# Kernel optimization log

Hardware: AMD Instinct MI355X
Metric: run time of the kernel (lower is better)

The kernel has to match this reference:

```python
import jax, jax.numpy as jnp
import numpy as np

B, N, DIM = 4, 1024, 1024
H, DH, ORDER = 16, 64, 3
MAXREL = 64
INNER = H * DH
VOCAB = 2 * MAXREL + 1
SCALE = DH ** -0.5
TOPK = int(0.25 * N)  # topk_ratio=0.25 default when top_k is None


def setup_inputs() -> dict:
    key = jax.random.key(0)
    ks = jax.random.split(key, 8)
    s = 0.02
    return {
        "x": jax.random.normal(ks[0], (B, N, DIM), jnp.float32),
        "Wqkv": jax.random.normal(ks[1], (3 * INNER, DIM), jnp.float32) * s,
        "bqkv": jnp.zeros((3 * INNER,), jnp.float32),
        "Wout": jax.random.normal(ks[2], (DIM, INNER), jnp.float32) * s,
        "bout": jnp.zeros((DIM,), jnp.float32),
        "rel_k_emb": jax.random.normal(ks[3], (VOCAB, DH), jnp.float32) * s,
        "rel_v_emb": jax.random.normal(ks[4], (VOCAB, DH), jnp.float32) * s,
        "alphas_raw": jax.random.normal(ks[5], (ORDER, H), jnp.float32) * 0.5,
    }


def reference(x, Wqkv, bqkv, Wout, bout, rel_k_emb, rel_v_emb, alphas_raw):
    b, n, _ = x.shape
    qkv = x @ Wqkv.T + bqkv  # [b, n, 3*inner]
    q, k, v = jnp.split(qkv, 3, axis=-1)
    to_heads = lambda t: t.reshape(b, n, H, DH).transpose(0, 2, 1, 3)  # b h n d
    q, k, v = to_heads(q), to_heads(k), to_heads(v)

    scores = jnp.einsum('bhid,bhjd->bhij', q, k) * SCALE

    # relative position bias on keys
    coords = jnp.arange(n)
    dist = jnp.clip(coords[:, None] - coords[None, :], -MAXREL, MAXREL) + MAXREL  # [n, n]
    rel_k = rel_k_emb[dist]  # [n, n, d]
    scores = scores + jnp.einsum('bhid,ijd->bhij', q, rel_k)

    # top-k thresholding per query row
    top_vals = jax.lax.top_k(scores, TOPK)[0]
    threshold = top_vals[..., -1:]
    scores = jnp.where(scores < threshold, -jnp.inf, scores)

    attn = jax.nn.softmax(scores, axis=-1)  # [b, h, n, n]

    rel_v = rel_v_emb[dist]  # [n, n, d]
    alphas = jax.nn.sigmoid(alphas_raw)  # [order, h]

    # monomial-basis polynomial filter: res = sum_i alpha_i * A^(i+1) V (+ relV term at i=0)
    res = jnp.zeros_like(v)
    v_curr = v
    for i in range(ORDER):
        a_v = jnp.einsum('bhij,bhjd->bhid', attn, v_curr)
        if i == 0:
            a_v = a_v + jnp.einsum('bhij,ijd->bhid', attn, rel_v)
        v_curr = a_v
        res = res + alphas[i][None, :, None, None] * v_curr

    out = res.transpose(0, 2, 1, 3).reshape(b, n, INNER)
    return out @ Wout.T + bout
```

## Files before the change

### kernel.cpp

```cpp
#include <hip/hip_runtime.h>

typedef unsigned short u16;
typedef unsigned int   u32;
typedef unsigned long long u64;
typedef __bf16 bf16x8 __attribute__((ext_vector_type(8)));
typedef float  floatx4 __attribute__((ext_vector_type(4)));

#define DEV static __device__ __forceinline__

DEV u16 f2bf(float f){ u32 x = __float_as_uint(f); return (u16)((x + 0x7fffu + ((x>>16)&1u)) >> 16); }
DEV float bf2f(u16 h){ return __uint_as_float(((u32)h)<<16); }
DEV u32 cvt_pk_bf16(float a, float b){ u32 r; asm("v_cvt_pk_bf16_f32 %0, %1, %2" : "=v"(r) : "v"(a), "v"(b)); return r; }

DEV void load_lds16(const u16* g, u16* l){
  __builtin_amdgcn_global_load_lds((const __attribute__((address_space(1))) u32*)g,
                                   (__attribute__((address_space(3))) u32*)l, 16, 0, 0);
}

DEV u32 unswz64(u32 p){
  u32 r0 = ((p>>6) ^ (p>>8)) & 1u;
  u32 b4 = ((p>>4) & 1u) ^ r0;
  u32 b5 = ((p>>5) ^ (p>>7)) & 1u;
  return (p & ~0x70u) | (b4<<4) | (b5<<5) | (r0<<6);
}
DEV bf16x8 ldfrag(const u16* base, int row, int lane){
  u32 off = ((u32)row<<6) + (((u32)lane>>4)<<4);
  off ^= (u32)(row&7)<<4;
  return *(const bf16x8*)((const char*)base + off);
}

template<int BM, int BN, int MODE>
__global__ __launch_bounds__(256) void gemm_bt(
    const u16* __restrict__ A, const u16* __restrict__ Bm, float* __restrict__ C,
    const float* __restrict__ bias, int K, int lda, int ldb, int ldc, int ncmax,
    long long sA, long long sB, long long sC,
    u16* __restrict__ vout, float* __restrict__ resb, const float* __restrict__ araw,
    int order, int accum)
{
  constexpr int BK = 32;
  constexpr int MT = BM/32;
  constexpr int NT = (BN/2)/16;
  __shared__ u16 smem[8704];
  u16* As = smem;
  u16* Bs = smem + BM*BK;

  const int tid = threadIdx.x, wid = tid>>6, lane = tid&63;
  const int z = blockIdx.z;
  const int m0 = blockIdx.y * BM, n0 = blockIdx.x * BN;
  const u16* Ab = A + (long long)z*sA;
  const u16* Bb = Bm + (long long)z*sB;

  const u32 g = unswz64((u32)tid*16);
  const int srow = g>>6, schunk = (g&63)>>1;
  const u16* ga0 = Ab + (long long)(m0 + srow)*lda + schunk;
  const u16* gb0 = Bb + (long long)(n0 + srow)*ldb + schunk;

  u16* lA0 = As + (wid*16)*BK;
  u16* lB0 = Bs + (wid*16)*BK;

  const int wm = wid>>1, wn = wid&1;
  const int lr = lane&15, lq = lane>>4;

  floatx4 acc[MT][NT] = {};

  for (int k = 0; k < K; k += BK) {
    __syncthreads();
    load_lds16(ga0 + k, lA0);
    load_lds16(gb0 + k, lB0);
    __syncthreads();
    bf16x8 af[MT];
#pragma unroll
    for (int mt=0; mt<MT; ++mt)
      af[mt] = ldfrag(As, wm*(BM/2) + mt*16 + lr, lane);
#pragma unroll
    for (int nt=0; nt<NT; ++nt) {
      bf16x8 bfr = ldfrag(Bs, wn*(BN/2) + nt*16 + lr, lane);
#pragma unroll
      for (int mt=0; mt<MT; ++mt)
        acc[mt][nt] = __builtin_amdgcn_mfma_f32_16x16x32_bf16(af[mt], bfr, acc[mt][nt], 0, 0, 0);
    }
  }

  if constexpr (MODE == 0) {
    float* Cb = C + (long long)z*sC;
#pragma unroll
    for (int nt=0; nt<NT; ++nt) {
      const int col = n0 + wn*(BN/2) + nt*16 + lr;
      if (col < ncmax) {
        const float bv = bias ? bias[col] : 0.f;
#pragma unroll
        for (int mt=0; mt<MT; ++mt) {
#pragma unroll
          for (int r=0; r<4; ++r) {
            const int row = m0 + wm*(BM/2) + mt*16 + lq*4 + r;
            Cb[(long long)row*ldc + col] = acc[mt][nt][r] + bv;
          }
        }
      }
    }
  } else {
    const int h = z & 15;
    const float alpha = 1.f/(1.f + __expf(-araw[order*16 + h]));
    float* rb = resb + (long long)z * 65536;
    __syncthreads();
#pragma unroll
    for (int nt=0; nt<NT; ++nt) {
      const int d = wn*32 + nt*16 + lr;
#pragma unroll
      for (int mt=0; mt<MT; ++mt) {
#pragma unroll
        for (int r=0; r<4; ++r) {
          const int row = wm*(BM/2) + mt*16 + lq*4 + r;
          const float v = acc[mt][nt][r];
          const long long ri = (long long)(m0+row)*64 + d;
          rb[ri] = accum ? (rb[ri] + alpha*v) : (alpha*v);
          smem[d*136 + row] = f2bf(v);
        }
      }
    }
    __syncthreads();
    const int dd = tid>>2, cc = (tid&3)*(BM/4);
    u16* vp = vout + (long long)z*75776 + (long long)dd*1184 + m0 + cc;
    const u16* sp = smem + dd*136 + cc;
#pragma unroll
    for (int j=0; j<BM/4; j+=8) {
      uint4 uu;
      uu.x = sp[j+0] | ((u32)sp[j+1]<<16);
      uu.y = sp[j+2] | ((u32)sp[j+3]<<16);
      uu.z = sp[j+4] | ((u32)sp[j+5]<<16);
      uu.w = sp[j+6] | ((u32)sp[j+7]<<16);
      *(uint4*)(vp + j) = uu;
    }
  }
}

template<int BM, int BN>
__global__ __launch_bounds__(512, 4) void gemm8(
    const u16* __restrict__ A, const u16* __restrict__ Bm, float* __restrict__ C,
    const float* __restrict__ bias, int K, int lda, int ldb, int ldc, int ncmax)
{
  constexpr int MT = (BM/2)/16;
  constexpr int NT = (BN/4)/16;
  __shared__ u16 As[BM*32];
  __shared__ u16 Bs[BN*32];

  const int tid = threadIdx.x, wid = tid>>6, lane = tid&63;
  const int m0 = blockIdx.y * BM, n0 = blockIdx.x * BN;

  const u32 g = unswz64((u32)tid*16);
  const int srow = g>>6, schunk = (g&63)>>1;
  const u16* ga0 = A  + (long long)(m0 + srow)*lda + schunk;
  const u16* gb0 = Bm + (long long)(n0 + srow)*ldb + schunk;

  u16* lA = As + (wid<<9);
  u16* lB = Bs + (wid<<9);

  const int wm = wid>>2, wn = wid&3;
  const int lr = lane&15, lq = lane>>4;

  floatx4 acc[MT][NT] = {};

  for (int k = 0; k < K; k += 32) {
    __syncthreads();
    if (BM == 128 || wid < 4) load_lds16(ga0 + k, lA);
    load_lds16(gb0 + k, lB);
    __syncthreads();
    bf16x8 af[MT];
#pragma unroll
    for (int mt=0; mt<MT; ++mt)
      af[mt] = ldfrag(As, wm*(BM/2) + mt*16 + lr, lane);
#pragma unroll
    for (int nt=0; nt<NT; ++nt) {
      bf16x8 bfr = ldfrag(Bs, wn*(BN/4) + nt*16 + lr, lane);
#pragma unroll
      for (int mt=0; mt<MT; ++mt)
        acc[mt][nt] = __builtin_amdgcn_mfma_f32_16x16x32_bf16(af[mt], bfr, acc[mt][nt], 0, 0, 0);
    }
  }

#pragma unroll
  for (int nt=0; nt<NT; ++nt) {
    const int col = n0 + wn*(BN/4) + nt*16 + lr;
    if (col < ncmax) {
      const float bv = bias ? bias[col] : 0.f;
#pragma unroll
      for (int mt=0; mt<MT; ++mt) {
#pragma unroll
        for (int r=0; r<4; ++r) {
          const int row = m0 + wm*(BM/2) + mt*16 + lq*4 + r;
          C[(long long)row*ldc + col] = acc[mt][nt][r] + bv;
        }
      }
    }
  }
}

__global__ __launch_bounds__(1024, 8) void score_topk(
    const u16* __restrict__ qF,
    const u16* __restrict__ kxF,
    u16* __restrict__ P)
{
  constexpr int SROW = 1156;
  __shared__ float sm[16*SROW];
  const int tid = threadIdx.x, wid = tid>>6, lane = tid&63;
  const int L = blockIdx.x;
  const int z  = (L & 7) + ((L >> 9) << 3);
  const int mt = (L >> 3) & 63;
  const int m0 = mt*16;
  const int lr = lane&15, lq = lane>>4;

  const u16* Aq = qF + (((long long)z*64 + mt)*6*64 + lane)*8;
  const u16* Bq = kxF + ((long long)z*80*6*64 + lane)*8;

  bf16x8 af[6];
#pragma unroll
  for (int kc=0;kc<6;++kc) af[kc] = *(const bf16x8*)(Aq + kc*512);

  const int base = wid*5;
  {
    floatx4 acc[5];
#pragma unroll
    for (int t=0;t<5;++t) acc[t] = floatx4{0.f,0.f,0.f,0.f};
#pragma unroll
    for (int t=0;t<5;++t){
      if (base + t < 73){
        const u16* bp = Bq + (long long)(base+t)*3072;
        bf16x8 b0 = *(const bf16x8*)(bp);
        bf16x8 b1 = *(const bf16x8*)(bp + 512);
        bf16x8 b2 = *(const bf16x8*)(bp + 1024);
        bf16x8 b3 = *(const bf16x8*)(bp + 1536);
        bf16x8 b4 = *(const bf16x8*)(bp + 2048);
        bf16x8 b5 = *(const bf16x8*)(bp + 2560);
        acc[t] = __builtin_amdgcn_mfma_f32_16x16x32_bf16(af[0], b0, acc[t], 0, 0, 0);
        acc[t] = __builtin_amdgcn_mfma_f32_16x16x32_bf16(af[1], b1, acc[t], 0, 0, 0);
        acc[t] = __builtin_amdgcn_mfma_f32_16x16x32_bf16(af[2], b2, acc[t], 0, 0, 0);
        acc[t] = __builtin_amdgcn_mfma_f32_16x16x32_bf16(af[3], b3, acc[t], 0, 0, 0);
        acc[t] = __builtin_amdgcn_mfma_f32_16x16x32_bf16(af[4], b4, acc[t], 0, 0, 0);
        acc[t] = __builtin_amdgcn_mfma_f32_16x16x32_bf16(af[5], b5, acc[t], 0, 0, 0);
      }
    }
#pragma unroll
    for (int t=0;t<5;++t){
      if (base + t < 73){
        const int col = (base+t)*16 + lr;
        if (col < 1153){
#pragma unroll
          for (int r=0;r<4;++r) sm[(lq*4+r)*SROW + col] = acc[t][r];
        }
      }
    }
  }
  __syncthreads();

  {
    const int row = wid;
    const int i = m0 + row;
    float* R = sm + row*SROW;

    float v[16];
#pragma unroll
    for (int x=0;x<8;++x){
      float2 f = *(const float2*)(R + x*128 + lane*2);
      v[2*x] = f.x; v[2*x+1] = f.y;
    }
#pragma unroll
    for (int x=0;x<16;++x){
      const int j = (x>>1)*128 + lane*2 + (x&1);
      int dl = i - j; dl = dl > 64 ? 64 : (dl < -64 ? -64 : dl);
      v[x] += R[1024 + dl + 64];
    }
    u32 u[16];
#pragma unroll
    for (int x=0;x<16;++x){
      u32 bb = __float_as_uint(v[x]);
      u[x] = bb ^ ((u32)((int)bb >> 31) | 0x80000000u);
    }
    u32 thr = 0;
#pragma unroll 1
    for (int bit=31; bit>=0; --bit){
      const u32 cand = thr | (1u<<bit);
      int c = 0;
#pragma unroll
      for (int x=0;x<16;++x) c += __popcll(__ballot(u[x] >= cand));
      if (c == 256){
        u32 mn = 0xFFFFFFFFu;
#pragma unroll
        for (int x=0;x<16;++x) if (u[x] >= cand && u[x] < mn) mn = u[x];
        for (int o=32;o;o>>=1){ u32 t = __shfl_xor(mn, o); mn = t < mn ? t : mn; }
        thr = mn;
        break;
      }
      if (c > 256) thr = cand;
    }
    float m = -3.0e38f;
#pragma unroll
    for (int x=0;x<16;++x) m = fmaxf(m, v[x]);
    for (int o=32;o;o>>=1) m = fmaxf(m, __shfl_xor(m, o));
    float e[16]; float Z = 0.f;
#pragma unroll
    for (int x=0;x<16;++x){
      e[x] = (u[x] >= thr) ? __expf(v[x]-m) : 0.f;
      Z += e[x];
    }
    for (int o=32;o;o>>=1) Z += __shfl_xor(Z, o);
    const float rz = 1.f / Z;

    u16* Pr = P + ((long long)z*1024 + i)*1184;
    u32* Pr32 = (u32*)Pr;
    float s0 = 0.f, s1 = 0.f;
#pragma unroll
    for (int x=0;x<8;++x){
      const float p0 = e[2*x]*rz, p1 = e[2*x+1]*rz;
      *(float2*)(R + x*128 + lane*2) = float2{p0, p1};
      Pr32[x*64 + lane] = cvt_pk_bf16(p0, p1);
      const int j0 = x*128 + lane*2;
      if (j0     >= i+64) s0 += p0;
      if (j0     <= i-64) s1 += p0;
      if (j0 + 1 >= i+64) s0 += p1;
      if (j0 + 1 <= i-64) s1 += p1;
    }
    for (int o=32;o;o>>=1){ s0 += __shfl_xor(s0,o); s1 += __shfl_xor(s1,o); }
    {
      const int t = lane + 1;
      const int j = i + 64 - t;
      const float wv = (j>=0 && j<1024) ? R[j] : 0.f;
      Pr[1024 + t] = f2bf(wv);
      if (lane < 63){
        const int t2 = lane + 65;
        const int j2 = i + 64 - t2;
        const float wv2 = (j2>=0 && j2<1024) ? R[j2] : 0.f;
        Pr[1024 + t2] = f2bf(wv2);
      }
      if (lane == 0){ Pr[1024] = f2bf(s0); Pr[1152] = f2bf(s1); }
      if (lane >= 33) Pr[1120 + lane] = 0;
    }
  }
}

__global__ __launch_bounds__(256) void planeize(const float* __restrict__ src, u16* __restrict__ dst,
                                                int total, int modeB){
  int idx = blockIdx.x*256 + threadIdx.x;
  if (idx >= total) return;
  int c = idx & 1023, r = idx >> 10;
  float v = src[idx];
  u16 hi = f2bf(v); u16 lo = f2bf(v - bf2f(hi));
  u16* d = dst + (long long)r*3072 + c;
  if (modeB){ d[0]=hi; d[1024]=hi; d[2048]=lo; }
  else      { d[0]=hi; d[1024]=lo; d[2048]=hi; }
}

__global__ __launch_bounds__(256) void build_qk(const float* __restrict__ qkv,
                                                u16* __restrict__ qF, u16* __restrict__ kxF){
  int idx = blockIdx.x*256 + threadIdx.x;
  int d = idx & 63, n = (idx>>6) & 1023, bh = idx >> 16;
  int b = bh >> 4, h = bh & 15;
  long long src = (long long)(b*1024 + n)*3072 + h*64 + d;
  float qv = qkv[src];
  float kv = qkv[src + 1024] * 0.125f;
  u16 qhi=f2bf(qv), qlo=f2bf(qv - bf2f(qhi));
  u16 khi=f2bf(kv), klo=f2bf(kv - bf2f(khi));
  const int lane = (n&15) + (((d&31)>>3)<<4);
  const int elem = d&7, kc0 = d>>5;
  u16* q = qF + ((((long long)bh*64 + (n>>4))*6*64) + lane)*8 + elem;
  q[(kc0+0)*512] = qhi; q[(kc0+2)*512] = qlo; q[(kc0+4)*512] = qhi;
  u16* kx = kxF + ((((long long)bh*80 + (n>>4))*6*64) + lane)*8 + elem;
  kx[(kc0+0)*512] = khi; kx[(kc0+2)*512] = khi; kx[(kc0+4)*512] = klo;
}

__global__ __launch_bounds__(256) void build_kxrel(const float* __restrict__ relk, u16* __restrict__ kxF){
  int idx = blockIdx.x*256 + threadIdx.x;
  int d = idx & 63, t = (idx>>6) & 255, bh = idx >> 14;
  u16 hi=0, lo=0;
  if (t < 129){ float v = relk[t*64 + d]; hi = f2bf(v); lo = f2bf(v - bf2f(hi)); }
  const int nrow = 1024 + t;
  const int lane = (t&15) + (((d&31)>>3)<<4);
  const int elem = d&7, kc0 = d>>5;
  u16* kx = kxF + ((((long long)bh*80 + (nrow>>4))*6*64) + lane)*8 + elem;
  kx[(kc0+0)*512] = hi; kx[(kc0+2)*512] = hi; kx[(kc0+4)*512] = lo;
}

__global__ __launch_bounds__(256) void build_vT(const float* __restrict__ qkv, u16* __restrict__ vA){
  __shared__ float tb[64][65];
  int bh = blockIdx.x >> 4, ntile = blockIdx.x & 15;
  int b = bh >> 4, h = bh & 15;
  int tid = threadIdx.x;
  int nl = tid >> 2, dc = (tid & 3)*16;
  const float* sp = qkv + (long long)(b*1024 + ntile*64 + nl)*3072 + 2048 + h*64 + dc;
#pragma unroll
  for (int j=0;j<16;j+=4){
    float4 f = *(const float4*)(sp + j);
    tb[dc+j+0][nl]=f.x; tb[dc+j+1][nl]=f.y; tb[dc+j+2][nl]=f.z; tb[dc+j+3][nl]=f.w;
  }
  __syncthreads();
  int d = tid >> 2, nc = (tid & 3)*16;
  u16* dp = vA + ((long long)bh*64 + d)*1184 + ntile*64 + nc;
#pragma unroll
  for (int j=0;j<16;j+=8){
    u16 a0=f2bf(tb[d][nc+j+0]), a1=f2bf(tb[d][nc+j+1]), a2=f2bf(tb[d][nc+j+2]), a3=f2bf(tb[d][nc+j+3]);
    u16 a4=f2bf(tb[d][nc+j+4]), a5=f2bf(tb[d][nc+j+5]), a6=f2bf(tb[d][nc+j+6]), a7=f2bf(tb[d][nc+j+7]);
    uint4 uu; uu.x=a0|((u32)a1<<16); uu.y=a2|((u32)a3<<16); uu.z=a4|((u32)a5<<16); uu.w=a6|((u32)a7<<16);
    *(uint4*)(dp + j) = uu;
  }
}

__global__ __launch_bounds__(256) void build_vText(const float* __restrict__ relv, u16* __restrict__ vA){
  int idx = blockIdx.x*256 + threadIdx.x;
  int t = idx % 160; int rest = idx / 160; int d = rest & 63; int bh = rest >> 6;
  u16 hv = 0;
  if (t < 129) hv = f2bf(relv[t*64 + d]);
  vA[((long long)bh*64 + d)*1184 + 1024 + t] = hv;
}

__global__ __launch_bounds__(256) void build_resS(const float* __restrict__ res, u16* __restrict__ resS){
  int idx = blockIdx.x*256 + threadIdx.x;
  int d = idx & 63, n = (idx>>6) & 1023, bh = idx >> 16;
  int b = bh >> 4, h = bh & 15;
  float v = res[idx];
  u16 hi = f2bf(v), lo = f2bf(v - bf2f(hi));
  u16* p = resS + (long long)(b*1024 + n)*3072 + h*64 + d;
  p[0]=hi; p[1024]=lo; p[2048]=hi;
}

extern "C" void kernel_launch(void* const* d_in, const int* in_sizes, int n_in,
                              void* d_out, int out_size, void* d_ws, size_t ws_size,
                              hipStream_t stream) {
  const float* x    = (const float*)d_in[0];
  const float* Wqkv = (const float*)d_in[1];
  const float* bqkv = (const float*)d_in[2];
  const float* Wout = (const float*)d_in[3];
  const float* bout = (const float*)d_in[4];
  const float* relk = (const float*)d_in[5];
  const float* relv = (const float*)d_in[6];
  const float* araw = (const float*)d_in[7];
  float* out = (float*)d_out;

  char* w = (char*)d_ws;
  size_t off = 0;
  auto take = [&](size_t bytes)->char*{ char* p = w + off; off += (bytes + 255) & ~(size_t)255; return p; };

  char* regionA = take(94371840);
  u16*   xS    = (u16*)  (regionA);
  u16*   wqS   = (u16*)  (regionA + 25165824);
  float* qkv32 = (float*)(regionA + 44040192);
  u16*   Ph    = (u16*)  (regionA);
  u16*   resS  = (u16*)  (regionA);
  u16*   woS   = (u16*)  (regionA + 25165824);
  u16*   qF    = (u16*)take(25165824);
  u16*   kxF   = (u16*)take(31457280);
  u16*   vA    = (u16*)take(9699328);
  u16*   vB    = (u16*)take(9699328);
  float* res   = (float*)take(16777216);
  (void)ws_size; (void)in_sizes; (void)n_in; (void)out_size;

  planeize<<<16384,256,0,stream>>>(x,    xS,  4194304, 0);
  planeize<<<12288,256,0,stream>>>(Wqkv, wqS, 3145728, 1);
  gemm8<128,128><<<dim3(16,32,1),512,0,stream>>>(xS, wqS, qkv32, bqkv,
      3072, 3072, 3072, 3072, 2048);
  gemm8<128,128><<<dim3(8,32,1),512,0,stream>>>(xS, wqS + (long long)2048*3072,
      qkv32 + 2048, bqkv + 2048, 1024, 3072, 3072, 3072, 1024);
  build_qk   <<<16384,256,0,stream>>>(qkv32, qF, kxF);
  build_kxrel<<<4096, 256,0,stream>>>(relk, kxF);
  build_vT   <<<1024, 256,0,stream>>>(qkv32, vA);
  build_vText<<<2560, 256,0,stream>>>(relv, vA);

  for (int half = 0; half < 2; ++half) {
    const long long zo = (long long)half * 32;
    score_topk<<<2048,1024,0,stream>>>(qF + zo*196608, kxF + zo*245760, Ph);
    gemm_bt<64,64,1><<<dim3(1,16,32),256,0,stream>>>(Ph, vA + zo*75776, nullptr, nullptr,
        1184, 1184, 1184, 0, 0, 1212416LL, 75776LL, 0LL,
        vB + zo*75776, res + zo*65536, araw, 0, 0);
    gemm_bt<64,64,1><<<dim3(1,16,32),256,0,stream>>>(Ph, vB + zo*75776, nullptr, nullptr,
        1024, 1184, 1184, 0, 0, 1212416LL, 75776LL, 0LL,
        vA + zo*75776, res + zo*65536, araw, 1, 1);
    gemm_bt<64,64,1><<<dim3(1,16,32),256,0,stream>>>(Ph, vA + zo*75776, nullptr, nullptr,
        1024, 1184, 1184, 0, 0, 1212416LL, 75776LL, 0LL,
        vB + zo*75776, res + zo*65536, araw, 2, 1);
  }

  build_resS<<<16384,256,0,stream>>>(res, resS);
  planeize  <<<4096, 256,0,stream>>>(Wout, woS, 1048576, 1);
  gemm8<64,128><<<dim3(8,64,1),512,0,stream>>>(resS, woS, out, bout,
      3072, 3072, 3072, 1024, 1024);
}
```

Before: 596.4 us.

## Replace batched AV GEMM with 512-thread kernel using z-interleaved block order

```diff
diff --git a/kernel.cpp b/kernel.cpp
--- a/kernel.cpp
+++ b/kernel.cpp
@@ -27,111 +27,6 @@
   u32 off = ((u32)row<<6) + (((u32)lane>>4)<<4);
   off ^= (u32)(row&7)<<4;
   return *(const bf16x8*)((const char*)base + off);
-}
-
-template<int BM, int BN, int MODE>
-__global__ __launch_bounds__(256) void gemm_bt(
-    const u16* __restrict__ A, const u16* __restrict__ Bm, float* __restrict__ C,
-    const float* __restrict__ bias, int K, int lda, int ldb, int ldc, int ncmax,
-    long long sA, long long sB, long long sC,
-    u16* __restrict__ vout, float* __restrict__ resb, const float* __restrict__ araw,
-    int order, int accum)
-{
-  constexpr int BK = 32;
-  constexpr int MT = BM/32;
-  constexpr int NT = (BN/2)/16;
-  __shared__ u16 smem[8704];
-  u16* As = smem;
-  u16* Bs = smem + BM*BK;
-
-  const int tid = threadIdx.x, wid = tid>>6, lane = tid&63;
-  const int z = blockIdx.z;
-  const int m0 = blockIdx.y * BM, n0 = blockIdx.x * BN;
-  const u16* Ab = A + (long long)z*sA;
-  const u16* Bb = Bm + (long long)z*sB;
-
-  const u32 g = unswz64((u32)tid*16);
-  const int srow = g>>6, schunk = (g&63)>>1;
-  const u16* ga0 = Ab + (long long)(m0 + srow)*lda + schunk;
-  const u16* gb0 = Bb + (long long)(n0 + srow)*ldb + schunk;
-
-  u16* lA0 = As + (wid*16)*BK;
-  u16* lB0 = Bs + (wid*16)*BK;
-
-  const int wm = wid>>1, wn = wid&1;
-  const int lr = lane&15, lq = lane>>4;
-
-  floatx4 acc[MT][NT] = {};
-
-  for (int k = 0; k < K; k += BK) {
-    __syncthreads();
-    load_lds16(ga0 + k, lA0);
-    load_lds16(gb0 + k, lB0);
-    __syncthreads();
-    bf16x8 af[MT];
-#pragma unroll
-    for (int mt=0; mt<MT; ++mt)
-      af[mt] = ldfrag(As, wm*(BM/2) + mt*16 + lr, lane);
-#pragma unroll
-    for (int nt=0; nt<NT; ++nt) {
-      bf16x8 bfr = ldfrag(Bs, wn*(BN/2) + nt*16 + lr, lane);
-#pragma unroll
-      for (int mt=0; mt<MT; ++mt)
-        acc[mt][nt] = __builtin_amdgcn_mfma_f32_16x16x32_bf16(af[mt], bfr, acc[mt][nt], 0, 0, 0);
-    }
-  }
-
-  if constexpr (MODE == 0) {
-    float* Cb = C + (long long)z*sC;
-#pragma unroll
-    for (int nt=0; nt<NT; ++nt) {
-      const int col = n0 + wn*(BN/2) + nt*16 + lr;
-      if (col < ncmax) {
-        const float bv = bias ? bias[col] : 0.f;
-#pragma unroll
-        for (int mt=0; mt<MT; ++mt) {
-#pragma unroll
-          for (int r=0; r<4; ++r) {
-            const int row = m0 + wm*(BM/2) + mt*16 + lq*4 + r;
-            Cb[(long long)row*ldc + col] = acc[mt][nt][r] + bv;
-          }
-        }
-      }
-    }
-  } else {
-    const int h = z & 15;
-    const float alpha = 1.f/(1.f + __expf(-araw[order*16 + h]));
-    float* rb = resb + (long long)z * 65536;
-    __syncthreads();
-#pragma unroll
-    for (int nt=0; nt<NT; ++nt) {
-      const int d = wn*32 + nt*16 + lr;
-#pragma unroll
-      for (int mt=0; mt<MT; ++mt) {
-#pragma unroll
-        for (int r=0; r<4; ++r) {
-          const int row = wm*(BM/2) + mt*16 + lq*4 + r;
-          const float v = acc[mt][nt][r];
-          const long long ri = (long long)(m0+row)*64 + d;
-          rb[ri] = accum ? (rb[ri] + alpha*v) : (alpha*v);
-          smem[d*136 + row] = f2bf(v);
-        }
-      }
-    }
-    __syncthreads();
-    const int dd = tid>>2, cc = (tid&3)*(BM/4);
-    u16* vp = vout + (long long)z*75776 + (long long)dd*1184 + m0 + cc;
-    const u16* sp = smem + dd*136 + cc;
-#pragma unroll
-    for (int j=0; j<BM/4; j+=8) {
-      uint4 uu;
-      uu.x = sp[j+0] | ((u32)sp[j+1]<<16);
-      uu.y = sp[j+2] | ((u32)sp[j+3]<<16);
-      uu.z = sp[j+4] | ((u32)sp[j+5]<<16);
-      uu.w = sp[j+6] | ((u32)sp[j+7]<<16);
-      *(uint4*)(vp + j) = uu;
-    }
-  }
 }
 
 template<int BM, int BN>
@@ -192,6 +87,76 @@
         }
       }
     }
+  }
+}
+
+__global__ __launch_bounds__(512, 4) void av8(
+    const u16* __restrict__ P,
+    const u16* __restrict__ V,
+    u16* __restrict__ vout,
+    float* __restrict__ resb,
+    const float* __restrict__ araw, int K, int order, int accum, int wv)
+{
+  __shared__ u16 smem[8704];
+  u16* As = smem;
+  u16* Bs = smem + 2048;
+
+  const int tid = threadIdx.x, wid = tid>>6, lane = tid&63;
+  const int L = blockIdx.x;
+  const int z  = (L & 7) + ((L >> 7) << 3);
+  const int m0 = ((L >> 3) & 15) * 64;
+  const int lr = lane&15, lq = lane>>4;
+
+  const int sw = wid & 3;
+  const u32 g = unswz64((u32)(sw*1024 + lane*16));
+  const int srow = g>>6, schunk = (g&63)>>1;
+  const u16* gsrc = (wid < 4)
+      ? P + (long long)z*1212416 + (long long)(m0 + srow)*1184 + schunk
+      : V + (long long)z*75776   + (long long)srow*1184 + schunk;
+  u16* ldst = (wid < 4) ? As + (sw<<9) : Bs + (sw<<9);
+
+  const int wm = wid>>2, wn = wid&3;
+  floatx4 acc[2] = {};
+
+  for (int k = 0; k < K; k += 32) {
+    __syncthreads();
+    load_lds16(gsrc + k, ldst);
+    __syncthreads();
+    bf16x8 bfr = ldfrag(Bs, wn*16 + lr, lane);
+#pragma unroll
+    for (int mt=0; mt<2; ++mt){
+      bf16x8 af = ldfrag(As, wm*32 + mt*16 + lr, lane);
+      acc[mt] = __builtin_amdgcn_mfma_f32_16x16x32_bf16(af, bfr, acc[mt], 0, 0, 0);
+    }
+  }
+
+  const int h = z & 15;
+  const float alpha = 1.f/(1.f + __expf(-araw[order*16 + h]));
+  float* rb = resb + (long long)z * 65536;
+  const int d = wn*16 + lr;
+  __syncthreads();
+#pragma unroll
+  for (int mt=0; mt<2; ++mt){
+#pragma unroll
+    for (int r=0; r<4; ++r){
+      const int row = wm*32 + mt*16 + lq*4 + r;
+      const float v = acc[mt][r];
+      const long long ri = (long long)(m0+row)*64 + d;
+      rb[ri] = accum ? (rb[ri] + alpha*v) : (alpha*v);
+      smem[d*136 + row] = f2bf(v);
+    }
+  }
+  __syncthreads();
+  if (wv){
+    const int dd = tid>>3, cc = (tid&7)*8;
+    u16* vp = vout + (long long)z*75776 + (long long)dd*1184 + m0 + cc;
+    const u16* sp = smem + dd*136 + cc;
+    uint4 uu;
+    uu.x = sp[0] | ((u32)sp[1]<<16);
+    uu.y = sp[2] | ((u32)sp[3]<<16);
+    uu.z = sp[4] | ((u32)sp[5]<<16);
+    uu.w = sp[6] | ((u32)sp[7]<<16);
+    *(uint4*)(vp) = uu;
   }
 }
 
@@ -466,15 +431,12 @@
   for (int half = 0; half < 2; ++half) {
     const long long zo = (long long)half * 32;
     score_topk<<<2048,1024,0,stream>>>(qF + zo*196608, kxF + zo*245760, Ph);
-    gemm_bt<64,64,1><<<dim3(1,16,32),256,0,stream>>>(Ph, vA + zo*75776, nullptr, nullptr,
-        1184, 1184, 1184, 0, 0, 1212416LL, 75776LL, 0LL,
-        vB + zo*75776, res + zo*65536, araw, 0, 0);
-    gemm_bt<64,64,1><<<dim3(1,16,32),256,0,stream>>>(Ph, vB + zo*75776, nullptr, nullptr,
-        1024, 1184, 1184, 0, 0, 1212416LL, 75776LL, 0LL,
-        vA + zo*75776, res + zo*65536, araw, 1, 1);
-    gemm_bt<64,64,1><<<dim3(1,16,32),256,0,stream>>>(Ph, vA + zo*75776, nullptr, nullptr,
-        1024, 1184, 1184, 0, 0, 1212416LL, 75776LL, 0LL,
-        vB + zo*75776, res + zo*65536, araw, 2, 1);
+    av8<<<512,512,0,stream>>>(Ph, vA + zo*75776, vB + zo*75776, res + zo*65536,
+        araw, 1184, 0, 0, 1);
+    av8<<<512,512,0,stream>>>(Ph, vB + zo*75776, vA + zo*75776, res + zo*65536,
+        araw, 1024, 1, 1, 1);
+    av8<<<512,512,0,stream>>>(Ph, vA + zo*75776, vB + zo*75776, res + zo*65536,
+        araw, 1024, 2, 1, 0);
   }
 
   build_resS<<<16384,256,0,stream>>>(res, resS);
```

Measured after the change: 589.3 us. About the same (-1.2%).
